# Kernel tuning notes

Measured on AMD Instinct MI355X. Metric: run time of the kernel, lower is better.

The kernel has to match this reference:

```python
import jax, jax.numpy as jnp
import numpy as np

B, G, F, H = 16, 128, 1024, 512
N = B * G  # graph size = batch_size * num_g_per_id
EPS = 1e-5
BN_SCALE = 1.0 / np.sqrt(1.0 + EPS)  # eval-mode BN with fresh running stats (mean 0, var 1)


def _bn(x, g, b):
    # nn.BatchNorm1d in eval mode with running_mean=0, running_var=1
    return g * (x * BN_SCALE) + b


def _lrelu(x):
    return jnp.where(x > 0, x, 0.1 * x)  # LeakyReLU(0.1)


def setup_inputs() -> dict:
    key = jax.random.key(0)
    ks = jax.random.split(key, 8)
    d = jax.random.normal(ks[0], (B, B, 1, G, F), dtype=jnp.float32)
    w = jax.random.uniform(ks[1], (N, N), dtype=jnp.float32)  # nonneg similarity graph
    label = jax.random.randint(ks[2], (B, B, 1, G), 0, 2, dtype=jnp.int64) if jax.config.read('jax_enable_x64') else jax.random.randint(ks[2], (B, B, 1, G), 0, 2, dtype=jnp.int32)
    def lin(k, i, o):
        return jax.random.normal(k, (i, o), dtype=jnp.float32) * (1.0 / np.sqrt(i))
    return {
        'd': d, 'w': w, 'label': label,
        'rf_W1': lin(ks[3], F, F), 'rf_b1': jnp.zeros((F,), jnp.float32),
        'rf_g1': jnp.ones((F,), jnp.float32), 'rf_be1': jnp.zeros((F,), jnp.float32),
        'rf_W2': lin(ks[4], F, F), 'rf_b2': jnp.zeros((F,), jnp.float32),
        'rf_g2': jnp.ones((F,), jnp.float32), 'rf_be2': jnp.zeros((F,), jnp.float32),
        'fc_W': lin(ks[5], F, H), 'fc_b': jnp.zeros((H,), jnp.float32),
        'fc_g': jnp.ones((H,), jnp.float32), 'fc_be': jnp.zeros((H,), jnp.float32),
        'cls_W': jax.random.normal(ks[6], (H, 1), jnp.float32) * 0.001,
        'cls_b': jnp.zeros((1,), jnp.float32),
    }


def reference(d, w, label, rf_W1, rf_b1, rf_g1, rf_be1, rf_W2, rf_b2, rf_g2, rf_be2,
              fc_W, fc_b, fc_g, fc_be, cls_W, cls_b):
    x = d.reshape(-1, F)
    x = _lrelu(_bn(x @ rf_W1 + rf_b1, rf_g1, rf_be1))
    x = _lrelu(_bn(x @ rf_W2 + rf_b2, rf_g2, rf_be2))
    t = x.reshape(B, N, F)  # [B, B*P*G, F] with P=1 -> [B, N, F]

    # Symmetric adjacency normalization: ((A+I) D^{-1/2})^T D^{-1/2}
    wa = w.reshape(N, N) + jnp.eye(N, dtype=w.dtype)
    dinv = jnp.power(wa.sum(axis=1), -0.5)
    dinv = jnp.where(jnp.isinf(dinv), 0.0, dinv)
    w_norm = (wa * dinv[None, :]).T * dinv[None, :]  # [N, N]

    # Graph propagation: d[:, :, f] = t[:, :, f] @ w_norm for every feature f
    dp = jnp.einsum('bnf,nm->bmf', t, w_norm)  # [B, N, F]

    # FcBlock + ClassBlock, vectorized over all (i, node) pairs
    y = dp.reshape(-1, F)
    y = _lrelu(_bn(y @ fc_W + fc_b, fc_g, fc_be))
    result = (y @ cls_W + cls_b).reshape(B, N)
    return result, label.reshape(B, -1)
```

## Files before the change

### kernel.cpp

```cpp
#include <hip/hip_runtime.h>

#define NN 2048
#define FD 1024
#define HD 512
#define MR 32768

typedef __attribute__((ext_vector_type(8))) short bf16x8;
typedef __attribute__((ext_vector_type(4))) float f32x4;

static constexpr float BNS = 0.99999500003749962f;

__device__ __forceinline__ float lrelu(float x) { return x > 0.f ? x : 0.1f * x; }

__device__ __forceinline__ unsigned short f2bf(float x) {
  unsigned u = __float_as_uint(x);
  u += 0x7fffu + ((u >> 16) & 1u);
  return (unsigned short)(u >> 16);
}
__device__ __forceinline__ float bf2f(unsigned short h) {
  return __uint_as_float(((unsigned)h) << 16);
}

__global__ __launch_bounds__(256) void split_rm(const float* __restrict__ src,
                                                unsigned short* __restrict__ hi,
                                                unsigned short* __restrict__ lo, int n4) {
  for (int i = blockIdx.x * 256 + threadIdx.x; i < n4; i += gridDim.x * 256) {
    float4 v = ((const float4*)src)[i];
    ushort4 h, l;
    h.x = f2bf(v.x); l.x = f2bf(v.x - bf2f(h.x));
    h.y = f2bf(v.y); l.y = f2bf(v.y - bf2f(h.y));
    h.z = f2bf(v.z); l.z = f2bf(v.z - bf2f(h.z));
    h.w = f2bf(v.w); l.w = f2bf(v.w - bf2f(h.w));
    ((ushort4*)hi)[i] = h;
    ((ushort4*)lo)[i] = l;
  }
}

__global__ __launch_bounds__(256) void split_w(const float* __restrict__ src,
                                               unsigned short* __restrict__ hi,
                                               unsigned short* __restrict__ lo) {
  for (int i = blockIdx.x * 256 + threadIdx.x; i < NN * NN / 4; i += gridDim.x * 256) {
    float4 v = ((const float4*)src)[i];
    const int e0 = i * 4;
    const int row = e0 >> 11;
    const int dcol = row - (e0 & (NN - 1));
    if (dcol == 0) v.x += 1.0f;
    else if (dcol == 1) v.y += 1.0f;
    else if (dcol == 2) v.z += 1.0f;
    else if (dcol == 3) v.w += 1.0f;
    ushort4 h, l;
    h.x = f2bf(v.x); l.x = f2bf(v.x - bf2f(h.x));
    h.y = f2bf(v.y); l.y = f2bf(v.y - bf2f(h.y));
    h.z = f2bf(v.z); l.z = f2bf(v.z - bf2f(h.z));
    h.w = f2bf(v.w); l.w = f2bf(v.w - bf2f(h.w));
    ((ushort4*)hi)[i] = h;
    ((ushort4*)lo)[i] = l;
  }
}

__global__ __launch_bounds__(256) void split_tr(const float* __restrict__ src,
                                                unsigned short* __restrict__ hi,
                                                unsigned short* __restrict__ lo,
                                                int K, int N) {
  __shared__ float t[32][33];
  const int n0 = blockIdx.x * 32, k0 = blockIdx.y * 32;
  const int tx = threadIdx.x & 31, ty = threadIdx.x >> 5;
  for (int i = ty; i < 32; i += 8) t[i][tx] = src[(size_t)(k0 + i) * N + n0 + tx];
  __syncthreads();
  for (int i = ty; i < 32; i += 8) {
    float v = t[tx][i];
    unsigned short h = f2bf(v);
    size_t o = (size_t)(n0 + i) * K + k0 + tx;
    hi[o] = h;
    lo[o] = f2bf(v - bf2f(h));
  }
}

__global__ __launch_bounds__(256) void dinv_kernel(const float* __restrict__ w,
                                                   float* __restrict__ dinv) {
  const int n = blockIdx.x;
  const float* row = w + (size_t)n * NN;
  float s = 0.f;
  for (int i = threadIdx.x; i < NN; i += 256) s += row[i];
#pragma unroll
  for (int off = 32; off > 0; off >>= 1) s += __shfl_down(s, off);
  __shared__ float red[4];
  const int lane = threadIdx.x & 63, wid = threadIdx.x >> 6;
  if (lane == 0) red[wid] = s;
  __syncthreads();
  if (threadIdx.x == 0) dinv[n] = 1.0f / sqrtf(red[0] + red[1] + red[2] + red[3] + 1.0f);
}

template <int EPI>
__global__ __launch_bounds__(256) void mfma_gemm(
    const unsigned short* __restrict__ Ah, const unsigned short* __restrict__ Al,
    const unsigned short* __restrict__ Bh, const unsigned short* __restrict__ Bl,
    const float* __restrict__ bias, const float* __restrict__ gam,
    const float* __restrict__ bet, const float* __restrict__ dinv,
    unsigned short* __restrict__ Ch, unsigned short* __restrict__ Cl,
    float* __restrict__ Cf, int M, int N, int K) {
  __shared__ unsigned short smem[4 * 4096];
  const char* smemc = (const char*)smem;
  const int tid = threadIdx.x;
  const int ln = tid & 63, wv = tid >> 6;
  const int wm = wv >> 1, wn = wv & 1;
  const int rowB = blockIdx.y * 128;
  const int colB = blockIdx.x * 128;
  const int z = (EPI == 2) ? blockIdx.z : 0;
  const size_t zB = (size_t)z * (size_t)N * (size_t)K;

  int srow[2], scol[2];
#pragma unroll
  for (int i = 0; i < 2; i++) {
    int q = (i * 4 + wv) * 64 + ln;
    int r = q >> 2, cp = q & 3;
    srow[i] = r;
    scol[i] = (cp ^ ((r >> 1) & 3)) * 8;
  }
  const unsigned short* gAh = Ah + (size_t)rowB * K;
  const unsigned short* gAl = Al + (size_t)rowB * K;
  const unsigned short* gBh = Bh + zB + (size_t)colB * K;
  const unsigned short* gBl = Bl + zB + (size_t)colB * K;

  const int lq = ln & 15, lg = ln >> 4;
  const int swz = (lg ^ ((lq >> 1) & 3)) * 16;
  const int aoff = lq * 64 + swz + wm * 4096;
  const int boff = lq * 64 + swz + wn * 4096;

  f32x4 acc[4][4] = {};

#define STAGE(gp, toff)                                                              \
  _Pragma("unroll") for (int i = 0; i < 2; i++) {                                    \
    __builtin_amdgcn_global_load_lds(                                                \
        (const __attribute__((address_space(1))) unsigned int*)((gp) +               \
            (size_t)srow[i] * K + scol[i] + k0),                                     \
        (__attribute__((address_space(3))) unsigned int*)((char*)smem + (toff) +     \
            (i * 4 + wv) * 1024),                                                    \
        16, 0, 0);                                                                   \
  }

  for (int k0 = 0; k0 < K; k0 += 32) {
    __syncthreads();
    STAGE(gAh, 0)
    STAGE(gAl, 8192)
    STAGE(gBh, 16384)
    STAGE(gBl, 24576)
    __syncthreads();

    bf16x8 fah[4], fal[4], fbh[4], fbl[4];
#pragma unroll
    for (int m = 0; m < 4; m++) {
      fah[m] = *(const bf16x8*)(smemc + 0 + aoff + m * 1024);
      fal[m] = *(const bf16x8*)(smemc + 8192 + aoff + m * 1024);
    }
#pragma unroll
    for (int n = 0; n < 4; n++) {
      fbh[n] = *(const bf16x8*)(smemc + 16384 + boff + n * 1024);
      fbl[n] = *(const bf16x8*)(smemc + 24576 + boff + n * 1024);
    }
#pragma unroll
    for (int m = 0; m < 4; m++)
#pragma unroll
      for (int n = 0; n < 4; n++) {
        acc[m][n] = __builtin_amdgcn_mfma_f32_16x16x32_bf16(fah[m], fbh[n], acc[m][n], 0, 0, 0);
        acc[m][n] = __builtin_amdgcn_mfma_f32_16x16x32_bf16(fah[m], fbl[n], acc[m][n], 0, 0, 0);
        acc[m][n] = __builtin_amdgcn_mfma_f32_16x16x32_bf16(fal[m], fbh[n], acc[m][n], 0, 0, 0);
      }
  }
#undef STAGE

  const int baseRow = rowB + wm * 64;
  const int baseCol = colB + wn * 64;

  if (EPI == 1) {
    unsigned short* ldsh = smem + wv * 1088;
    unsigned short* ldsl = smem + 4352 + wv * 1088;
    const int b = baseRow >> 11;
    const int nodeB = baseRow & (NN - 1);
#pragma unroll
    for (int n = 0; n < 4; n++) {
      __syncthreads();
      const int gcol = baseCol + n * 16 + lq;
      const float bi = bias[gcol], ga = gam[gcol], be = bet[gcol];
#pragma unroll
      for (int m = 0; m < 4; m++)
#pragma unroll
        for (int r = 0; r < 4; r++) {
          const int row = m * 16 + lg * 4 + r;
          float v = acc[m][n][r] + bi;
          v = ga * (v * BNS) + be;
          v = lrelu(v) * dinv[(baseRow + row) & (NN - 1)];
          unsigned short h = f2bf(v);
          ldsh[lq * 68 + row] = h;
          ldsl[lq * 68 + row] = f2bf(v - bf2f(h));
        }
      __syncthreads();
#pragma unroll
      for (int it = 0; it < 4; it++) {
        const int c = it * 4 + lg;
        const int rr = lq * 4;
        ushort4 hv = *(const ushort4*)&ldsh[c * 68 + rr];
        ushort4 lv = *(const ushort4*)&ldsl[c * 68 + rr];
        const size_t o = (size_t)b * ((size_t)N * NN) +
                         (size_t)(baseCol + n * 16 + c) * NN + (nodeB + rr);
        *(ushort4*)&Ch[o] = hv;
        *(ushort4*)&Cl[o] = lv;
      }
    }
    return;
  }

#pragma unroll
  for (int m = 0; m < 4; m++) {
#pragma unroll
    for (int n = 0; n < 4; n++) {
#pragma unroll
      for (int r = 0; r < 4; r++) {
        const int row = baseRow + m * 16 + lg * 4 + r;
        const int col = baseCol + n * 16 + lq;
        float v = acc[m][n][r];
        if (EPI == 0 || EPI == 3) {
          v += bias[col];
          v = gam[col] * (v * BNS) + bet[col];
          v = lrelu(v);
        }
        if (EPI == 0) {
          unsigned short h = f2bf(v);
          size_t o = (size_t)row * N + col;
          Ch[o] = h;
          Cl[o] = f2bf(v - bf2f(h));
        } else if (EPI == 2) {
          v = dinv[row] * v;
          unsigned short h = f2bf(v);
          size_t o = ((size_t)z * NN + row) * (size_t)N + col;
          Ch[o] = h;
          Cl[o] = f2bf(v - bf2f(h));
        } else if (EPI == 3) {
          Cf[(size_t)row * N + col] = v;
        }
      }
    }
  }
}

__global__ __launch_bounds__(256) void cls_kernel(const float* __restrict__ Y,
                                                  const float* __restrict__ clsW,
                                                  const float* __restrict__ clsb,
                                                  float* __restrict__ out) {
  const int gid = blockIdx.x * 256 + threadIdx.x;
  const int wave = gid >> 6, lane = gid & 63;
  const float* y = Y + (size_t)wave * HD;
  float s = 0.f;
#pragma unroll
  for (int i = 0; i < HD / 64; i++) s += y[lane + i * 64] * clsW[lane + i * 64];
#pragma unroll
  for (int off = 32; off > 0; off >>= 1) s += __shfl_down(s, off);
  if (lane == 0) out[wave] = s + clsb[0];
}

__global__ __launch_bounds__(256) void label_kernel(const int* __restrict__ lab,
                                                    float* __restrict__ out) {
  const int i = blockIdx.x * 256 + threadIdx.x;
  out[i] = (float)lab[i];
}

extern "C" void kernel_launch(void* const* d_in, const int* in_sizes, int n_in,
                              void* d_out, int out_size, void* d_ws, size_t ws_size,
                              hipStream_t stream) {
  const float* d      = (const float*)d_in[0];
  const float* w      = (const float*)d_in[1];
  const int*   label  = (const int*)d_in[2];
  const float* rf_W1  = (const float*)d_in[3];
  const float* rf_b1  = (const float*)d_in[4];
  const float* rf_g1  = (const float*)d_in[5];
  const float* rf_be1 = (const float*)d_in[6];
  const float* rf_W2  = (const float*)d_in[7];
  const float* rf_b2  = (const float*)d_in[8];
  const float* rf_g2  = (const float*)d_in[9];
  const float* rf_be2 = (const float*)d_in[10];
  const float* fc_W   = (const float*)d_in[11];
  const float* fc_b   = (const float*)d_in[12];
  const float* fc_g   = (const float*)d_in[13];
  const float* fc_be  = (const float*)d_in[14];
  const float* cls_W  = (const float*)d_in[15];
  const float* cls_b  = (const float*)d_in[16];

  float* out = (float*)d_out;
  char* ws = (char*)d_ws;
  const size_t MB = 1024ull * 1024ull;
  unsigned short* R0h = (unsigned short*)(ws);
  unsigned short* R0l = (unsigned short*)(ws + 64 * MB);
  unsigned short* R1h = (unsigned short*)(ws + 128 * MB);
  unsigned short* R1l = (unsigned short*)(ws + 192 * MB);
  unsigned short* wh  = (unsigned short*)(ws + 256 * MB);
  unsigned short* wl  = (unsigned short*)(ws + 264 * MB);
  unsigned short* W1th = (unsigned short*)(ws + 272 * MB);
  unsigned short* W1tl = (unsigned short*)(ws + 274 * MB);
  unsigned short* W2th = (unsigned short*)(ws + 276 * MB);
  unsigned short* W2tl = (unsigned short*)(ws + 278 * MB);
  unsigned short* fcth = (unsigned short*)(ws + 280 * MB);
  unsigned short* fctl = (unsigned short*)(ws + 281 * MB);
  float* dinvp = (float*)(ws + 282 * MB);
  float* Yf = (float*)(ws);

  split_rm<<<2048, 256, 0, stream>>>(d, R0h, R0l, MR * FD / 4);
  split_w<<<1024, 256, 0, stream>>>(w, wh, wl);
  split_tr<<<dim3(FD / 32, FD / 32), 256, 0, stream>>>(rf_W1, W1th, W1tl, FD, FD);
  split_tr<<<dim3(FD / 32, FD / 32), 256, 0, stream>>>(rf_W2, W2th, W2tl, FD, FD);
  split_tr<<<dim3(HD / 32, FD / 32), 256, 0, stream>>>(fc_W, fcth, fctl, FD, HD);
  dinv_kernel<<<NN, 256, 0, stream>>>(w, dinvp);

  mfma_gemm<0><<<dim3(FD / 128, MR / 128), 256, 0, stream>>>(
      R0h, R0l, W1th, W1tl, rf_b1, rf_g1, rf_be1, nullptr, R1h, R1l, nullptr, MR, FD, FD);
  mfma_gemm<1><<<dim3(FD / 128, MR / 128), 256, 0, stream>>>(
      R1h, R1l, W2th, W2tl, rf_b2, rf_g2, rf_be2, dinvp, R0h, R0l, nullptr, MR, FD, FD);
  mfma_gemm<2><<<dim3(FD / 128, NN / 128, 16), 256, 0, stream>>>(
      wh, wl, R0h, R0l, nullptr, nullptr, nullptr, dinvp, R1h, R1l, nullptr, NN, FD, NN);
  mfma_gemm<3><<<dim3(HD / 128, MR / 128), 256, 0, stream>>>(
      R1h, R1l, fcth, fctl, fc_b, fc_g, fc_be, nullptr, nullptr, nullptr, Yf, MR, HD, FD);
  cls_kernel<<<MR / 4, 256, 0, stream>>>(Yf, cls_W, cls_b, out);
  label_kernel<<<MR / 256, 256, 0, stream>>>(label, out + MR);
}
```

Before: 1.263 ms.

## Double GEMM K-tile to 64 and fuse classifier into final GEMM epilogue

Each shared-memory K stage now loads 64 elements instead of 32, with a new 8-way XOR swizzle, and shared memory grows to 64KB. This halves the number of barrier pairs per GEMM. The classifier dot product moves into the epilogue of the last GEMM: each wave applies BN and LeakyReLU, does a shuffle reduction, and atomically adds into an output that a new init kernel pre-fills with the bias and labels. This removes the fp32 Y buffer round trip and the separate cls and label kernels, at the cost of lower occupancy from the larger LDS and float atomics whose summation order varies between runs.

```diff
diff --git a/kernel.cpp b/kernel.cpp
--- a/kernel.cpp
+++ b/kernel.cpp
@@ -91,6 +91,14 @@
   if (threadIdx.x == 0) dinv[n] = 1.0f / sqrtf(red[0] + red[1] + red[2] + red[3] + 1.0f);
 }
 
+__global__ __launch_bounds__(256) void init_out(const int* __restrict__ lab,
+                                                const float* __restrict__ clsb,
+                                                float* __restrict__ out) {
+  const int i = blockIdx.x * 256 + threadIdx.x;
+  if (i < MR) out[i] = clsb[0];
+  else out[i] = (float)lab[i - MR];
+}
+
 template <int EPI>
 __global__ __launch_bounds__(256) void mfma_gemm(
     const unsigned short* __restrict__ Ah, const unsigned short* __restrict__ Al,
@@ -98,8 +106,9 @@
     const float* __restrict__ bias, const float* __restrict__ gam,
     const float* __restrict__ bet, const float* __restrict__ dinv,
     unsigned short* __restrict__ Ch, unsigned short* __restrict__ Cl,
-    float* __restrict__ Cf, int M, int N, int K) {
-  __shared__ unsigned short smem[4 * 4096];
+    const float* __restrict__ clsW, float* __restrict__ outF,
+    int M, int N, int K) {
+  __shared__ unsigned short smem[4 * 8192];
   const char* smemc = (const char*)smem;
   const int tid = threadIdx.x;
   const int ln = tid & 63, wv = tid >> 6;
@@ -109,13 +118,13 @@
   const int z = (EPI == 2) ? blockIdx.z : 0;
   const size_t zB = (size_t)z * (size_t)N * (size_t)K;
 
-  int srow[2], scol[2];
-#pragma unroll
-  for (int i = 0; i < 2; i++) {
-    int q = (i * 4 + wv) * 64 + ln;
-    int r = q >> 2, cp = q & 3;
-    srow[i] = r;
-    scol[i] = (cp ^ ((r >> 1) & 3)) * 8;
+  int srow[4], scol[4];
+#pragma unroll
+  for (int it = 0; it < 4; it++) {
+    int q = it * 256 + tid;
+    int r = q >> 3, cp = q & 7;
+    srow[it] = r;
+    scol[it] = (cp ^ (r & 7)) * 8;
   }
   const unsigned short* gAh = Ah + (size_t)rowB * K;
   const unsigned short* gAl = Al + (size_t)rowB * K;
@@ -123,49 +132,52 @@
   const unsigned short* gBl = Bl + zB + (size_t)colB * K;
 
   const int lq = ln & 15, lg = ln >> 4;
-  const int swz = (lg ^ ((lq >> 1) & 3)) * 16;
-  const int aoff = lq * 64 + swz + wm * 4096;
-  const int boff = lq * 64 + swz + wn * 4096;
+  const int arow = (wm * 64 + lq) * 128;
+  const int brow = (wn * 64 + lq) * 128;
 
   f32x4 acc[4][4] = {};
 
 #define STAGE(gp, toff)                                                              \
-  _Pragma("unroll") for (int i = 0; i < 2; i++) {                                    \
+  _Pragma("unroll") for (int it = 0; it < 4; it++) {                                 \
     __builtin_amdgcn_global_load_lds(                                                \
         (const __attribute__((address_space(1))) unsigned int*)((gp) +               \
-            (size_t)srow[i] * K + scol[i] + k0),                                     \
+            (size_t)srow[it] * K + scol[it] + k0),                                   \
         (__attribute__((address_space(3))) unsigned int*)((char*)smem + (toff) +     \
-            (i * 4 + wv) * 1024),                                                    \
+            it * 4096 + wv * 1024),                                                  \
         16, 0, 0);                                                                   \
   }
 
-  for (int k0 = 0; k0 < K; k0 += 32) {
+  for (int k0 = 0; k0 < K; k0 += 64) {
     __syncthreads();
     STAGE(gAh, 0)
-    STAGE(gAl, 8192)
-    STAGE(gBh, 16384)
-    STAGE(gBl, 24576)
+    STAGE(gAl, 16384)
+    STAGE(gBh, 32768)
+    STAGE(gBl, 49152)
     __syncthreads();
 
-    bf16x8 fah[4], fal[4], fbh[4], fbl[4];
-#pragma unroll
-    for (int m = 0; m < 4; m++) {
-      fah[m] = *(const bf16x8*)(smemc + 0 + aoff + m * 1024);
-      fal[m] = *(const bf16x8*)(smemc + 8192 + aoff + m * 1024);
+#pragma unroll
+    for (int kk = 0; kk < 2; kk++) {
+      const int cs = ((kk * 4 + lg) ^ (lq & 7)) * 16;
+      bf16x8 fah[4], fal[4], fbh[4], fbl[4];
+#pragma unroll
+      for (int m = 0; m < 4; m++) {
+        fah[m] = *(const bf16x8*)(smemc + 0 + arow + m * 2048 + cs);
+        fal[m] = *(const bf16x8*)(smemc + 16384 + arow + m * 2048 + cs);
+      }
+#pragma unroll
+      for (int n = 0; n < 4; n++) {
+        fbh[n] = *(const bf16x8*)(smemc + 32768 + brow + n * 2048 + cs);
+        fbl[n] = *(const bf16x8*)(smemc + 49152 + brow + n * 2048 + cs);
+      }
+#pragma unroll
+      for (int m = 0; m < 4; m++)
+#pragma unroll
+        for (int n = 0; n < 4; n++) {
+          acc[m][n] = __builtin_amdgcn_mfma_f32_16x16x32_bf16(fah[m], fbh[n], acc[m][n], 0, 0, 0);
+          acc[m][n] = __builtin_amdgcn_mfma_f32_16x16x32_bf16(fah[m], fbl[n], acc[m][n], 0, 0, 0);
+          acc[m][n] = __builtin_amdgcn_mfma_f32_16x16x32_bf16(fal[m], fbh[n], acc[m][n], 0, 0, 0);
+        }
     }
-#pragma unroll
-    for (int n = 0; n < 4; n++) {
-      fbh[n] = *(const bf16x8*)(smemc + 16384 + boff + n * 1024);
-      fbl[n] = *(const bf16x8*)(smemc + 24576 + boff + n * 1024);
-    }
-#pragma unroll
-    for (int m = 0; m < 4; m++)
-#pragma unroll
-      for (int n = 0; n < 4; n++) {
-        acc[m][n] = __builtin_amdgcn_mfma_f32_16x16x32_bf16(fah[m], fbh[n], acc[m][n], 0, 0, 0);
-        acc[m][n] = __builtin_amdgcn_mfma_f32_16x16x32_bf16(fah[m], fbl[n], acc[m][n], 0, 0, 0);
-        acc[m][n] = __builtin_amdgcn_mfma_f32_16x16x32_bf16(fal[m], fbh[n], acc[m][n], 0, 0, 0);
-      }
   }
 #undef STAGE
 
@@ -210,6 +222,34 @@
     return;
   }
 
+  if (EPI == 3) {
+    float bi[4], ga[4], be[4], cw[4];
+#pragma unroll
+    for (int n = 0; n < 4; n++) {
+      const int col = baseCol + n * 16 + lq;
+      bi[n] = bias[col]; ga[n] = gam[col]; be[n] = bet[col]; cw[n] = clsW[col];
+    }
+#pragma unroll
+    for (int m = 0; m < 4; m++)
+#pragma unroll
+      for (int r = 0; r < 4; r++) {
+        const int row = baseRow + m * 16 + lg * 4 + r;
+        float part = 0.f;
+#pragma unroll
+        for (int n = 0; n < 4; n++) {
+          float v = acc[m][n][r] + bi[n];
+          v = ga[n] * (v * BNS) + be[n];
+          part += lrelu(v) * cw[n];
+        }
+        part += __shfl_xor(part, 1);
+        part += __shfl_xor(part, 2);
+        part += __shfl_xor(part, 4);
+        part += __shfl_xor(part, 8);
+        if (lq == 0) atomicAdd(&outF[row], part);
+      }
+    return;
+  }
+
 #pragma unroll
   for (int m = 0; m < 4; m++) {
 #pragma unroll
@@ -219,12 +259,10 @@
         const int row = baseRow + m * 16 + lg * 4 + r;
         const int col = baseCol + n * 16 + lq;
         float v = acc[m][n][r];
-        if (EPI == 0 || EPI == 3) {
+        if (EPI == 0) {
           v += bias[col];
           v = gam[col] * (v * BNS) + bet[col];
           v = lrelu(v);
-        }
-        if (EPI == 0) {
           unsigned short h = f2bf(v);
           size_t o = (size_t)row * N + col;
           Ch[o] = h;
@@ -235,33 +273,10 @@
           size_t o = ((size_t)z * NN + row) * (size_t)N + col;
           Ch[o] = h;
           Cl[o] = f2bf(v - bf2f(h));
-        } else if (EPI == 3) {
-          Cf[(size_t)row * N + col] = v;
         }
       }
     }
   }
-}
-
-__global__ __launch_bounds__(256) void cls_kernel(const float* __restrict__ Y,
-                                                  const float* __restrict__ clsW,
-                                                  const float* __restrict__ clsb,
-                                                  float* __restrict__ out) {
-  const int gid = blockIdx.x * 256 + threadIdx.x;
-  const int wave = gid >> 6, lane = gid & 63;
-  const float* y = Y + (size_t)wave * HD;
-  float s = 0.f;
-#pragma unroll
-  for (int i = 0; i < HD / 64; i++) s += y[lane + i * 64] * clsW[lane + i * 64];
-#pragma unroll
-  for (int off = 32; off > 0; off >>= 1) s += __shfl_down(s, off);
-  if (lane == 0) out[wave] = s + clsb[0];
-}
-
-__global__ __launch_bounds__(256) void label_kernel(const int* __restrict__ lab,
-                                                    float* __restrict__ out) {
-  const int i = blockIdx.x * 256 + threadIdx.x;
-  out[i] = (float)lab[i];
 }
 
 extern "C" void kernel_launch(void* const* d_in, const int* in_sizes, int n_in,
@@ -301,7 +316,6 @@
   unsigned short* fcth = (unsigned short*)(ws + 280 * MB);
   unsigned short* fctl = (unsigned short*)(ws + 281 * MB);
   float* dinvp = (float*)(ws + 282 * MB);
-  float* Yf = (float*)(ws);
 
   split_rm<<<2048, 256, 0, stream>>>(d, R0h, R0l, MR * FD / 4);
   split_w<<<1024, 256, 0, stream>>>(w, wh, wl);
@@ -309,15 +323,18 @@
   split_tr<<<dim3(FD / 32, FD / 32), 256, 0, stream>>>(rf_W2, W2th, W2tl, FD, FD);
   split_tr<<<dim3(HD / 32, FD / 32), 256, 0, stream>>>(fc_W, fcth, fctl, FD, HD);
   dinv_kernel<<<NN, 256, 0, stream>>>(w, dinvp);
+  init_out<<<2 * MR / 256, 256, 0, stream>>>(label, cls_b, out);
 
   mfma_gemm<0><<<dim3(FD / 128, MR / 128), 256, 0, stream>>>(
-      R0h, R0l, W1th, W1tl, rf_b1, rf_g1, rf_be1, nullptr, R1h, R1l, nullptr, MR, FD, FD);
+      R0h, R0l, W1th, W1tl, rf_b1, rf_g1, rf_be1, nullptr, R1h, R1l, nullptr, nullptr,
+      MR, FD, FD);
   mfma_gemm<1><<<dim3(FD / 128, MR / 128), 256, 0, stream>>>(
-      R1h, R1l, W2th, W2tl, rf_b2, rf_g2, rf_be2, dinvp, R0h, R0l, nullptr, MR, FD, FD);
+      R1h, R1l, W2th, W2tl, rf_b2, rf_g2, rf_be2, dinvp, R0h, R0l, nullptr, nullptr,
+      MR, FD, FD);
   mfma_gemm<2><<<dim3(FD / 128, NN / 128, 16), 256, 0, stream>>>(
-      wh, wl, R0h, R0l, nullptr, nullptr, nullptr, dinvp, R1h, R1l, nullptr, NN, FD, NN);
+      wh, wl, R0h, R0l, nullptr, nullptr, nullptr, dinvp, R1h, R1l, nullptr, nullptr,
+      NN, FD, NN);
   mfma_gemm<3><<<dim3(HD / 128, MR / 128), 256, 0, stream>>>(
-      R1h, R1l, fcth, fctl, fc_b, fc_g, fc_be, nullptr, nullptr, nullptr, Yf, MR, HD, FD);
-  cls_kernel<<<MR / 4, 256, 0, stream>>>(Yf, cls_W, cls_b, out);
-  label_kernel<<<MR / 256, 256, 0, stream>>>(label, out + MR);
-}
+      R1h, R1l, fcth, fctl, fc_b, fc_g, fc_be, nullptr, nullptr, nullptr, cls_W, out,
+      MR, HD, FD);
+}
```

Result: faster. 1.094 ms (-13.4%).
